# Performance work log

Hardware: AMD Instinct MI355X
Metric: run time of the kernel (lower is better)

## Reference

```python
import jax, jax.numpy as jnp
import numpy as np

N, F, H, E, R = 100000, 256, 64, 800000, 7
EPS = 1e-5

def _layernorm(x, g, b):
    mu = jnp.mean(x, axis=-1, keepdims=True)
    var = jnp.mean((x - mu) ** 2, axis=-1, keepdims=True)
    return (x - mu) * jax.lax.rsqrt(var + EPS) * g + b

def setup_inputs() -> dict:
    key = jax.random.key(0)
    ks = jax.random.split(key, 16)
    block_features = jax.random.normal(ks[0], (N, F), dtype=jnp.float32)
    src = jax.random.randint(ks[1], (E,), 0, N).astype(jnp.float32)
    dst = jax.random.randint(ks[2], (E,), 0, N).astype(jnp.float32)
    rel = jax.random.randint(ks[3], (E,), 0, R).astype(jnp.float32)
    w = jax.random.uniform(ks[4], (E,), dtype=jnp.float32)
    typed_edges = jnp.stack([src, dst, rel, w], axis=1)  # [E,4]
    def lin(k, fan_in, fan_out):
        s = 1.0 / np.sqrt(fan_in)
        k1, k2 = jax.random.split(k)
        return (jax.random.uniform(k1, (fan_in, fan_out), jnp.float32, -s, s),
                jax.random.uniform(k2, (fan_out,), jnp.float32, -s, s))
    W1, b1 = lin(ks[5], F, H)
    W2, b2 = lin(ks[6], H, H)
    rel_emb = jax.random.normal(ks[7], (R, H), dtype=jnp.float32)
    Wm1, bm1 = lin(ks[8], 3 * H + 1, H)
    Wm2, bm2 = lin(ks[9], H, H)
    Wg1, bg1 = lin(ks[10], 2 * H, H)
    Wg2, bg2 = lin(ks[11], H, H)
    return dict(block_features=block_features, typed_edges=typed_edges,
                W1=W1, b1=b1, g1=jnp.ones(H), be1=jnp.zeros(H), W2=W2, b2=b2,
                rel_emb=rel_emb, Wm1=Wm1, bm1=bm1, Wm2=Wm2, bm2=bm2,
                gn=jnp.ones(H), bn=jnp.zeros(H), Wg1=Wg1, bg1=bg1, Wg2=Wg2, bg2=bg2)

def reference(block_features, typed_edges, W1, b1, g1, be1, W2, b2, rel_emb,
              Wm1, bm1, Wm2, bm2, gn, bn, Wg1, bg1, Wg2, bg2):
    # node_proj: Linear -> LN -> ReLU -> Linear -> ReLU
    h = jax.nn.relu(_layernorm(block_features @ W1 + b1, g1, be1))
    h = jax.nn.relu(h @ W2 + b2)  # [N,H]
    src = typed_edges[:, 0].astype(jnp.int32)
    dst = typed_edges[:, 1].astype(jnp.int32)
    rel = typed_edges[:, 2].astype(jnp.int32)
    w = typed_edges[:, 3:4]  # [E,1]
    m_in = jnp.concatenate([h[src], h[dst], rel_emb[rel], w], axis=-1)  # [E,3H+1]
    msg = jax.nn.relu(m_in @ Wm1 + bm1) @ Wm2 + bm2  # [E,H]
    agg = jax.ops.segment_sum(msg, dst, num_segments=h.shape[0])  # [N,H]
    nodes = _layernorm(h + agg, gn, bn)
    g = jnp.concatenate([nodes.mean(axis=0), nodes.max(axis=0)], axis=-1)  # [2H]
    return jax.nn.relu(g @ Wg1 + bg1) @ Wg2 + bg2  # [H]
```

## Files before the change

kernel.cpp:

```cpp
#include <hip/hip_runtime.h>

typedef unsigned short u16;
typedef unsigned int   u32;
typedef __attribute__((ext_vector_type(8))) short bf16x8;
typedef __attribute__((ext_vector_type(4))) float f32x4;

#define EPS 1e-5f
#define MFMA(a,b,c) __builtin_amdgcn_mfma_f32_16x16x32_bf16(a,b,c,0,0,0)

constexpr int OB_b1=0, OB_g1=64, OB_be1=128, OB_b2=192, OB_bm1=256, OB_w192=320,
              OB_bm2=384, OB_gn=448, OB_bn=512, OB_bg1=576, OB_bg2=640,
              OB_Wg1=704, OB_Wg2=8896, WB_TOT=12992;
constexpr int FR_Wm1=0;
constexpr int FR_Wm2=12288;
constexpr int FR_rel=16384;
constexpr int FR_W1 =16960;
constexpr int FR_W2 =33344;
constexpr int FR_TOT=37440;

__device__ __forceinline__ float bf2f(u32 u) { return __uint_as_float(u << 16); }
__device__ __forceinline__ u16 f2bf(float f) {
  u32 b = __float_as_uint(f);
  return (u16)((b + 0x7fffu + ((b >> 16) & 1u)) >> 16);
}
__device__ __forceinline__ u32 fkey(float f) {
  u32 b = __float_as_uint(f);
  return (b & 0x80000000u) ? ~b : (b | 0x80000000u);
}

__launch_bounds__(256)
__global__ void k_prep(const float* __restrict__ W1, const float* __restrict__ b1,
                       const float* __restrict__ g1, const float* __restrict__ be1,
                       const float* __restrict__ W2, const float* __restrict__ b2,
                       const float* __restrict__ rel_emb,
                       const float* __restrict__ Wm1, const float* __restrict__ bm1,
                       const float* __restrict__ Wm2, const float* __restrict__ bm2,
                       const float* __restrict__ gn, const float* __restrict__ bn,
                       const float* __restrict__ Wg1, const float* __restrict__ bg1,
                       const float* __restrict__ Wg2, const float* __restrict__ bg2,
                       float* __restrict__ wbuf, u16* __restrict__ frags) {
  int tid = blockIdx.x * 256 + threadIdx.x;
  int nth = gridDim.x * 256;
  for (int i = tid; i < 64; i += nth) {
    wbuf[OB_b1 + i] = b1[i];   wbuf[OB_g1 + i] = g1[i];
    wbuf[OB_be1 + i] = be1[i]; wbuf[OB_b2 + i] = b2[i];
    wbuf[OB_bm1 + i] = bm1[i]; wbuf[OB_w192 + i] = Wm1[192 * 64 + i];
    wbuf[OB_bm2 + i] = bm2[i]; wbuf[OB_gn + i] = gn[i];
    wbuf[OB_bn + i] = bn[i];   wbuf[OB_bg1 + i] = bg1[i];
    wbuf[OB_bg2 + i] = bg2[i];
  }
  for (int i = tid; i < 8192; i += nth) wbuf[OB_Wg1 + i] = Wg1[i];
  for (int i = tid; i < 4096; i += nth) wbuf[OB_Wg2 + i] = Wg2[i];
  for (int idx = tid; idx < 16384; idx += nth) {
    int f = idx >> 9, L = (idx >> 3) & 63, j = idx & 7;
    int k = (f >> 2) * 32 + ((L >> 4) << 3) + j, n = ((f & 3) << 4) + (L & 15);
    frags[FR_W1 + idx] = f2bf(W1[k * 64 + n]);
  }
  for (int idx = tid; idx < 4096; idx += nth) {
    int f = idx >> 9, L = (idx >> 3) & 63, j = idx & 7;
    int k = (f >> 2) * 32 + ((L >> 4) << 3) + j, n = ((f & 3) << 4) + (L & 15);
    frags[FR_W2 + idx] = f2bf(W2[k * 64 + n]);
  }
  for (int idx = tid; idx < 12288; idx += nth) {
    int f = idx >> 9, L = (idx >> 3) & 63, j = idx & 7;
    int k = (f >> 2) * 32 + ((L >> 4) << 3) + j, n = ((f & 3) << 4) + (L & 15);
    frags[FR_Wm1 + idx] = f2bf(Wm1[k * 64 + n]);
  }
  for (int idx = tid; idx < 4096; idx += nth) {
    int f = idx >> 9, L = (idx >> 3) & 63, j = idx & 7;
    int k = (f >> 2) * 32 + ((L >> 4) << 3) + j, n = ((f & 3) << 4) + (L & 15);
    frags[FR_Wm2 + idx] = f2bf(Wm2[k * 64 + n]);
  }
  for (int idx = tid; idx < 576; idx += nth) {
    int r = idx / 80, c = idx % 80;
    frags[FR_rel + idx] = (r < 7 && c < 64) ? f2bf(rel_emb[r * 64 + c]) : (u16)0;
  }
}

__launch_bounds__(256, 3)
__global__ void k_h(const float* __restrict__ X, const float* __restrict__ wbuf,
                    const u16* __restrict__ frags, u16* __restrict__ hb, int N) {
  __shared__ __align__(16) u16 sW1[32 * 512];
  __shared__ __align__(16) u16 sW2[8 * 512];
  __shared__ __align__(16) u16 st[4][16 * 72];

  {
    const uint4* srcp = (const uint4*)(frags + FR_W1);
    uint4* d1 = (uint4*)sW1;
    for (int i = threadIdx.x; i < 2048; i += 256) d1[i] = srcp[i];
    const uint4* srcp2 = (const uint4*)(frags + FR_W2);
    uint4* d2 = (uint4*)sW2;
    for (int i = threadIdx.x; i < 512; i += 256) d2[i] = srcp2[i];
  }
  __syncthreads();

  int lane = threadIdx.x & 63, wave = threadIdx.x >> 6;
  int m = lane & 15, quad = lane >> 4, koff = quad * 8, col0 = m;

  float b1v[4], g1v[4], be1v[4], b2v[4];
  #pragma unroll
  for (int nt = 0; nt < 4; nt++) {
    int c = nt * 16 + col0;
    b1v[nt] = wbuf[OB_b1 + c]; g1v[nt] = wbuf[OB_g1 + c];
    be1v[nt] = wbuf[OB_be1 + c]; b2v[nt] = wbuf[OB_b2 + c];
  }

  int ntiles = (N + 15) / 16;
  int wid = blockIdx.x * 4 + wave, nw = gridDim.x * 4;
  for (int tile = wid; tile < ntiles; tile += nw) {
    int n0 = tile * 16;
    int nm = min(n0 + m, N - 1);
    const float* xr = X + (size_t)nm * 256 + koff;

    f32x4 acc[4] = {};
    #pragma unroll 1
    for (int ks = 0; ks < 8; ks++) {
      float4 u0 = *(const float4*)(xr + ks * 32);
      float4 u1 = *(const float4*)(xr + ks * 32 + 4);
      bf16x8 a;
      a[0] = (short)f2bf(u0.x); a[1] = (short)f2bf(u0.y);
      a[2] = (short)f2bf(u0.z); a[3] = (short)f2bf(u0.w);
      a[4] = (short)f2bf(u1.x); a[5] = (short)f2bf(u1.y);
      a[6] = (short)f2bf(u1.z); a[7] = (short)f2bf(u1.w);
      #pragma unroll
      for (int nt = 0; nt < 4; nt++) {
        bf16x8 b = *(const bf16x8*)(sW1 + (ks * 4 + nt) * 512 + lane * 8);
        acc[nt] = MFMA(a, b, acc[nt]);
      }
    }

    float v[4][4];
    #pragma unroll
    for (int nt = 0; nt < 4; nt++)
      #pragma unroll
      for (int r = 0; r < 4; r++) v[nt][r] = acc[nt][r] + b1v[nt];

    #pragma unroll
    for (int r = 0; r < 4; r++) {
      float s = v[0][r] + v[1][r] + v[2][r] + v[3][r];
      #pragma unroll
      for (int mk = 8; mk >= 1; mk >>= 1) s += __shfl_xor(s, mk, 64);
      float mu = s * (1.f / 64.f);
      float q = 0.f;
      #pragma unroll
      for (int nt = 0; nt < 4; nt++) { float d = v[nt][r] - mu; q += d * d; }
      #pragma unroll
      for (int mk = 8; mk >= 1; mk >>= 1) q += __shfl_xor(q, mk, 64);
      float rs = rsqrtf(q * (1.f / 64.f) + EPS);
      #pragma unroll
      for (int nt = 0; nt < 4; nt++) {
        float h1 = fmaxf(fmaf((v[nt][r] - mu) * rs, g1v[nt], be1v[nt]), 0.f);
        st[wave][(quad * 4 + r) * 72 + nt * 16 + col0] = f2bf(h1);
      }
    }
    __builtin_amdgcn_wave_barrier();

    f32x4 acc2[4] = {};
    #pragma unroll
    for (int ks = 0; ks < 2; ks++) {
      bf16x8 a2 = *(const bf16x8*)(st[wave] + m * 72 + ks * 32 + koff);
      #pragma unroll
      for (int nt = 0; nt < 4; nt++) {
        bf16x8 b = *(const bf16x8*)(sW2 + (ks * 4 + nt) * 512 + lane * 8);
        acc2[nt] = MFMA(a2, b, acc2[nt]);
      }
    }
    __builtin_amdgcn_wave_barrier();

    #pragma unroll
    for (int nt = 0; nt < 4; nt++)
      #pragma unroll
      for (int r = 0; r < 4; r++) {
        int row = n0 + quad * 4 + r;
        if (row < N)
          hb[(size_t)row * 64 + nt * 16 + col0] = f2bf(fmaxf(acc2[nt][r] + b2v[nt], 0.f));
      }
  }
}

__launch_bounds__(256, 3)
__global__ void k_edge(const float* __restrict__ te, const u16* __restrict__ hb,
                       const float* __restrict__ wbuf, const u16* __restrict__ frags,
                       float* __restrict__ agg, int E, int N) {
  __shared__ __align__(16) u16 sWm1[24 * 512];
  __shared__ __align__(16) u16 sWm2[8 * 512];
  __shared__ __align__(16) u16 srel[576];
  __shared__ __align__(16) u16 st[4][16 * 72];

  {
    const uint4* s1 = (const uint4*)(frags + FR_Wm1);
    uint4* d1 = (uint4*)sWm1;
    for (int i = threadIdx.x; i < 1536; i += 256) d1[i] = s1[i];
    const uint4* s2 = (const uint4*)(frags + FR_Wm2);
    uint4* d2 = (uint4*)sWm2;
    for (int i = threadIdx.x; i < 512; i += 256) d2[i] = s2[i];
    const uint4* s3 = (const uint4*)(frags + FR_rel);
    uint4* d3 = (uint4*)srel;
    for (int i = threadIdx.x; i < 72; i += 256) d3[i] = s3[i];
  }
  __syncthreads();

  int lane = threadIdx.x & 63, wave = threadIdx.x >> 6;
  int m = lane & 15, quad = lane >> 4, koff = quad * 8, col0 = m;

  float bm1v[4], w192v[4], bm2v[4];
  #pragma unroll
  for (int nt = 0; nt < 4; nt++) {
    int c = nt * 16 + col0;
    bm1v[nt] = wbuf[OB_bm1 + c];
    w192v[nt] = wbuf[OB_w192 + c];
    bm2v[nt] = wbuf[OB_bm2 + c];
  }

  int ntiles = (E + 15) / 16;
  int wid = blockIdx.x * 4 + wave, nw = gridDim.x * 4;
  for (int tile = wid; tile < ntiles; tile += nw) {
    int e0 = tile * 16;
    int src = 0, dst = 0, rel = 0; float w = 0.f;
    if (lane < 16) {
      int e = min(e0 + lane, E - 1);
      float4 v = *(const float4*)(te + (size_t)e * 4);
      src = min(max((int)v.x, 0), N - 1);
      dst = min(max((int)v.y, 0), N - 1);
      rel = min(max((int)v.z, 0), 6);
      w = v.w;
    }
    int src_m = __shfl(src, m, 64);
    int dst_m = __shfl(dst, m, 64);
    int rel_m = __shfl(rel, m, 64);

    const u16* hs = hb + (size_t)src_m * 64;
    const u16* hd = hb + (size_t)dst_m * 64;
    bf16x8 af[6];
    af[0] = *(const bf16x8*)(hs + koff);
    af[1] = *(const bf16x8*)(hs + 32 + koff);
    af[2] = *(const bf16x8*)(hd + koff);
    af[3] = *(const bf16x8*)(hd + 32 + koff);
    af[4] = *(const bf16x8*)(srel + rel_m * 80 + koff);
    af[5] = *(const bf16x8*)(srel + rel_m * 80 + 32 + koff);

    f32x4 acc[4] = {};
    #pragma unroll
    for (int ks = 0; ks < 6; ks++) {
      #pragma unroll
      for (int nt = 0; nt < 4; nt++) {
        bf16x8 b = *(const bf16x8*)(sWm1 + (ks * 4 + nt) * 512 + lane * 8);
        acc[nt] = MFMA(af[ks], b, acc[nt]);
      }
    }

    float wrow[4];
    #pragma unroll
    for (int r = 0; r < 4; r++) wrow[r] = __shfl(w, quad * 4 + r, 64);
    #pragma unroll
    for (int nt = 0; nt < 4; nt++)
      #pragma unroll
      for (int r = 0; r < 4; r++) {
        float v = fmaf(wrow[r], w192v[nt], acc[nt][r] + bm1v[nt]);
        st[wave][(quad * 4 + r) * 72 + nt * 16 + col0] = f2bf(fmaxf(v, 0.f));
      }
    __builtin_amdgcn_wave_barrier();

    f32x4 acc2[4] = {};
    #pragma unroll
    for (int ks = 0; ks < 2; ks++) {
      bf16x8 a2 = *(const bf16x8*)(st[wave] + m * 72 + ks * 32 + koff);
      #pragma unroll
      for (int nt = 0; nt < 4; nt++) {
        bf16x8 b = *(const bf16x8*)(sWm2 + (ks * 4 + nt) * 512 + lane * 8);
        acc2[nt] = MFMA(a2, b, acc2[nt]);
      }
    }
    __builtin_amdgcn_wave_barrier();

    int dstr[4]; bool valr[4];
    #pragma unroll
    for (int r = 0; r < 4; r++) {
      int row = quad * 4 + r;
      dstr[r] = __shfl(dst, row, 64);
      valr[r] = (e0 + row) < E;
    }
    #pragma unroll
    for (int nt = 0; nt < 4; nt++)
      #pragma unroll
      for (int r = 0; r < 4; r++)
        if (valr[r])
          atomicAdd(agg + (size_t)dstr[r] * 64 + nt * 16 + col0, acc2[nt][r] + bm2v[nt]);
  }
}

__launch_bounds__(256)
__global__ void k_nodes(const u16* __restrict__ hb, const float* __restrict__ agg,
                        const float* __restrict__ wbuf, float* __restrict__ gsum,
                        u32* __restrict__ gmax, int N) {
  int lane = threadIdx.x & 63, wave = threadIdx.x >> 6;
  int wid = blockIdx.x * 4 + wave;
  int nw = gridDim.x * 4;
  float gn = wbuf[OB_gn + lane], bn = wbuf[OB_bn + lane];
  float sj = 0.f, mj = -3.0e38f;
  for (int n = wid; n < N; n += nw) {
    float v = bf2f(hb[(size_t)n * 64 + lane]) + agg[(size_t)n * 64 + lane];
    float s = v;
    #pragma unroll
    for (int m = 32; m >= 1; m >>= 1) s += __shfl_xor(s, m, 64);
    float mu = s * (1.f / 64.f);
    float d = v - mu;
    float q = d * d;
    #pragma unroll
    for (int m = 32; m >= 1; m >>= 1) q += __shfl_xor(q, m, 64);
    float rs = rsqrtf(q * (1.f / 64.f) + EPS);
    float val = fmaf(d * rs, gn, bn);
    sj += val;
    mj = fmaxf(mj, val);
  }
  __shared__ float bs[256], bm[256];
  bs[threadIdx.x] = sj;
  bm[threadIdx.x] = mj;
  __syncthreads();
  if (threadIdx.x < 64) {
    int t = threadIdx.x;
    float ts = bs[t] + bs[64 + t] + bs[128 + t] + bs[192 + t];
    float tm = fmaxf(fmaxf(bm[t], bm[64 + t]), fmaxf(bm[128 + t], bm[192 + t]));
    atomicAdd(gsum + t, ts);
    atomicMax(gmax + t, fkey(tm));
  }
}

__launch_bounds__(128)
__global__ void k_final(const float* __restrict__ wbuf, const float* __restrict__ gsum,
                        const u32* __restrict__ gmax, float* __restrict__ out, int N) {
  __shared__ float g[128];
  __shared__ float y1[64];
  int t = threadIdx.x;
  if (t < 64) {
    g[t] = gsum[t] / (float)N;
  } else {
    u32 k = gmax[t - 64];
    u32 b = (k & 0x80000000u) ? (k & 0x7fffffffu) : ~k;
    g[t] = __uint_as_float(b);
  }
  __syncthreads();
  if (t < 64) {
    float a = wbuf[OB_bg1 + t];
    for (int i = 0; i < 128; i++) a = fmaf(g[i], wbuf[OB_Wg1 + i * 64 + t], a);
    y1[t] = fmaxf(a, 0.f);
  }
  __syncthreads();
  if (t < 64) {
    float a = wbuf[OB_bg2 + t];
    for (int k = 0; k < 64; k++) a = fmaf(y1[k], wbuf[OB_Wg2 + k * 64 + t], a);
    out[t] = a;
  }
}

extern "C" void kernel_launch(void* const* d_in, const int* in_sizes, int n_in,
                              void* d_out, int out_size, void* d_ws, size_t ws_size,
                              hipStream_t stream) {
  const int N = in_sizes[0] / 256;
  const int E = in_sizes[1] / 4;

  char* ws = (char*)d_ws;
  size_t aggB = (size_t)N * 64 * 4;
  size_t hbB  = (size_t)N * 64 * 2;
  float* agg   = (float*)ws;
  u16*   hb    = (u16*)(ws + aggB);
  float* gsum  = (float*)(ws + aggB + hbB);
  u32*   gmax  = (u32*)(ws + aggB + hbB + 256);
  float* wbuf  = (float*)(ws + aggB + hbB + 512);
  u16*   frags = (u16*)(ws + aggB + hbB + 512 + (size_t)WB_TOT * 4);

  const float* X  = (const float*)d_in[0];
  const float* te = (const float*)d_in[1];

  hipLaunchKernelGGL(k_prep, dim3(64), dim3(256), 0, stream,
                     (const float*)d_in[2], (const float*)d_in[3], (const float*)d_in[4],
                     (const float*)d_in[5], (const float*)d_in[6], (const float*)d_in[7],
                     (const float*)d_in[8], (const float*)d_in[9], (const float*)d_in[10],
                     (const float*)d_in[11], (const float*)d_in[12], (const float*)d_in[13],
                     (const float*)d_in[14], (const float*)d_in[15], (const float*)d_in[16],
                     (const float*)d_in[17], (const float*)d_in[18], wbuf, frags);
  hipMemsetAsync(agg, 0, aggB, stream);
  hipMemsetAsync(gsum, 0, 512, stream);
  hipLaunchKernelGGL(k_h, dim3(640), dim3(256), 0, stream, X, wbuf, frags, hb, N);
  hipLaunchKernelGGL(k_edge, dim3(768), dim3(256), 0, stream, te, hb, wbuf, frags, agg, E, N);
  hipLaunchKernelGGL(k_nodes, dim3(2048), dim3(256), 0, stream, hb, agg, wbuf, gsum, gmax, N);
  hipLaunchKernelGGL(k_final, dim3(1), dim3(128), 0, stream, wbuf, gsum, gmax, (float*)d_out, N);
}
```

Before: 442.6 us.

## Sort edges by destination and reduce messages per segment before atomics

Adds a counting sort of edges by destination: a count pass in the prep kernel, a three-kernel scan and a permutation kernel. The edge kernel then walks sorted ranges of 128 edges, adding up messages for each destination inside the wave. It writes interior segments with plain stores and uses atomics only for segments that touch a range boundary. The goal is to cut the roughly 64 fp32 atomics issued per edge. In exchange it adds extra launches, random reads of the edge table through the permutation, a serial 16-row reduction loop, and rounding of message outputs to bf16 before they are summed. It also unrolls the node-projection K loop and changes grid sizes.

```diff
diff --git a/kernel.cpp b/kernel.cpp
--- a/kernel.cpp
+++ b/kernel.cpp
@@ -38,7 +38,9 @@
                        const float* __restrict__ gn, const float* __restrict__ bn,
                        const float* __restrict__ Wg1, const float* __restrict__ bg1,
                        const float* __restrict__ Wg2, const float* __restrict__ bg2,
-                       float* __restrict__ wbuf, u16* __restrict__ frags) {
+                       float* __restrict__ wbuf, u16* __restrict__ frags,
+                       const float* __restrict__ te, u32* __restrict__ counts,
+                       int E, int N) {
   int tid = blockIdx.x * 256 + threadIdx.x;
   int nth = gridDim.x * 256;
   for (int i = tid; i < 64; i += nth) {
@@ -75,6 +77,76 @@
     int r = idx / 80, c = idx % 80;
     frags[FR_rel + idx] = (r < 7 && c < 64) ? f2bf(rel_emb[r * 64 + c]) : (u16)0;
   }
+  for (int e = tid; e < E; e += nth) {
+    float dv = te[(size_t)e * 4 + 1];
+    int d = min(max((int)dv, 0), N - 1);
+    atomicAdd(&counts[d], 1u);
+  }
+}
+
+__launch_bounds__(256)
+__global__ void k_scan1(const u32* __restrict__ counts, u32* __restrict__ partial, int M) {
+  __shared__ u32 red[256];
+  int base = blockIdx.x * 1024;
+  u32 s = 0;
+  #pragma unroll
+  for (int k = 0; k < 4; k++) { int i = base + threadIdx.x + k * 256; if (i < M) s += counts[i]; }
+  red[threadIdx.x] = s; __syncthreads();
+  for (int off = 128; off > 0; off >>= 1) {
+    if (threadIdx.x < (u32)off) red[threadIdx.x] += red[threadIdx.x + off];
+    __syncthreads();
+  }
+  if (threadIdx.x == 0) partial[blockIdx.x] = red[0];
+}
+
+__launch_bounds__(256)
+__global__ void k_scan2(u32* __restrict__ partial, int PB) {
+  __shared__ u32 sh[1024];
+  for (int i = threadIdx.x; i < PB; i += 256) sh[i] = partial[i];
+  __syncthreads();
+  if (threadIdx.x == 0) {
+    u32 acc = 0;
+    for (int i = 0; i < PB; i++) { u32 t = sh[i]; sh[i] = acc; acc += t; }
+  }
+  __syncthreads();
+  for (int i = threadIdx.x; i < PB; i += 256) partial[i] = sh[i];
+}
+
+__launch_bounds__(256)
+__global__ void k_scan3(const u32* __restrict__ counts, const u32* __restrict__ partial,
+                        u32* __restrict__ offsets, u32* __restrict__ cursor, int M) {
+  __shared__ u32 tsum[256];
+  int base = blockIdx.x * 1024 + threadIdx.x * 4;
+  u32 c[4]; u32 s = 0;
+  #pragma unroll
+  for (int k = 0; k < 4; k++) { int i = base + k; c[k] = (i < M) ? counts[i] : 0u; s += c[k]; }
+  tsum[threadIdx.x] = s; __syncthreads();
+  for (int off = 1; off < 256; off <<= 1) {
+    u32 v = (threadIdx.x >= (u32)off) ? tsum[threadIdx.x - off] : 0u;
+    __syncthreads();
+    tsum[threadIdx.x] += v;
+    __syncthreads();
+  }
+  u32 excl = (threadIdx.x == 0) ? 0u : tsum[threadIdx.x - 1];
+  u32 run = partial[blockIdx.x] + excl;
+  #pragma unroll
+  for (int k = 0; k < 4; k++) {
+    int i = base + k;
+    if (i < M) { offsets[i] = run; cursor[i] = run; run += c[k]; }
+  }
+}
+
+__launch_bounds__(256)
+__global__ void k_perm(const float* __restrict__ te, u32* __restrict__ cursor,
+                       u32* __restrict__ perm, int E, int N) {
+  int tid = blockIdx.x * 256 + threadIdx.x;
+  int nth = gridDim.x * 256;
+  for (int e = tid; e < E; e += nth) {
+    float dv = te[(size_t)e * 4 + 1];
+    int d = min(max((int)dv, 0), N - 1);
+    u32 pos = atomicAdd(&cursor[d], 1u);
+    perm[pos] = (u32)e;
+  }
 }
 
 __launch_bounds__(256, 3)
@@ -113,7 +185,7 @@
     const float* xr = X + (size_t)nm * 256 + koff;
 
     f32x4 acc[4] = {};
-    #pragma unroll 1
+    #pragma unroll 4
     for (int ks = 0; ks < 8; ks++) {
       float4 u0 = *(const float4*)(xr + ks * 32);
       float4 u1 = *(const float4*)(xr + ks * 32 + 4);
@@ -179,13 +251,15 @@
 }
 
 __launch_bounds__(256, 3)
-__global__ void k_edge(const float* __restrict__ te, const u16* __restrict__ hb,
-                       const float* __restrict__ wbuf, const u16* __restrict__ frags,
-                       float* __restrict__ agg, int E, int N) {
+__global__ void k_edge(const float* __restrict__ te, const u32* __restrict__ perm,
+                       const u16* __restrict__ hb, const float* __restrict__ wbuf,
+                       const u16* __restrict__ frags, float* __restrict__ agg,
+                       int E, int N, int nranges) {
   __shared__ __align__(16) u16 sWm1[24 * 512];
   __shared__ __align__(16) u16 sWm2[8 * 512];
   __shared__ __align__(16) u16 srel[576];
   __shared__ __align__(16) u16 st[4][16 * 72];
+  __shared__ int ldst[4][16];
 
   {
     const uint4* s1 = (const uint4*)(frags + FR_Wm1);
@@ -212,80 +286,105 @@
     bm2v[nt] = wbuf[OB_bm2 + c];
   }
 
-  int ntiles = (E + 15) / 16;
   int wid = blockIdx.x * 4 + wave, nw = gridDim.x * 4;
-  for (int tile = wid; tile < ntiles; tile += nw) {
-    int e0 = tile * 16;
-    int src = 0, dst = 0, rel = 0; float w = 0.f;
-    if (lane < 16) {
-      int e = min(e0 + lane, E - 1);
-      float4 v = *(const float4*)(te + (size_t)e * 4);
-      src = min(max((int)v.x, 0), N - 1);
-      dst = min(max((int)v.y, 0), N - 1);
-      rel = min(max((int)v.z, 0), 6);
-      w = v.w;
+  for (int range = wid; range < nranges; range += nw) {
+    int r0 = range * 128;
+    int run_dst = -2;
+    float run = 0.f;
+    bool bs = false;
+
+    #pragma unroll 1
+    for (int t8 = 0; t8 < 8; t8++) {
+      int p0 = r0 + t8 * 16;
+      if (p0 >= E) break;
+
+      int src = 0, dstc = 0, rel = 0, dtag = -1; float w = 0.f;
+      if (lane < 16) {
+        int p = p0 + lane;
+        if (p < E) {
+          u32 eid = perm[p];
+          float4 v = *(const float4*)(te + (size_t)eid * 4);
+          src = min(max((int)v.x, 0), N - 1);
+          dstc = min(max((int)v.y, 0), N - 1);
+          rel = min(max((int)v.z, 0), 6);
+          w = v.w;
+          dtag = dstc;
+        }
+        ldst[wave][lane] = dtag;
+      }
+      int src_m = __shfl(src, m, 64);
+      int dst_m = __shfl(dstc, m, 64);
+      int rel_m = __shfl(rel, m, 64);
+
+      const u16* hs = hb + (size_t)src_m * 64;
+      const u16* hd = hb + (size_t)dst_m * 64;
+      bf16x8 af[6];
+      af[0] = *(const bf16x8*)(hs + koff);
+      af[1] = *(const bf16x8*)(hs + 32 + koff);
+      af[2] = *(const bf16x8*)(hd + koff);
+      af[3] = *(const bf16x8*)(hd + 32 + koff);
+      af[4] = *(const bf16x8*)(srel + rel_m * 80 + koff);
+      af[5] = *(const bf16x8*)(srel + rel_m * 80 + 32 + koff);
+
+      f32x4 acc[4] = {};
+      #pragma unroll
+      for (int ks = 0; ks < 6; ks++) {
+        #pragma unroll
+        for (int nt = 0; nt < 4; nt++) {
+          bf16x8 b = *(const bf16x8*)(sWm1 + (ks * 4 + nt) * 512 + lane * 8);
+          acc[nt] = MFMA(af[ks], b, acc[nt]);
+        }
+      }
+
+      float wrow[4];
+      #pragma unroll
+      for (int r = 0; r < 4; r++) wrow[r] = __shfl(w, quad * 4 + r, 64);
+      #pragma unroll
+      for (int nt = 0; nt < 4; nt++)
+        #pragma unroll
+        for (int r = 0; r < 4; r++) {
+          float v = fmaf(wrow[r], w192v[nt], acc[nt][r] + bm1v[nt]);
+          st[wave][(quad * 4 + r) * 72 + nt * 16 + col0] = f2bf(fmaxf(v, 0.f));
+        }
+      __builtin_amdgcn_wave_barrier();
+
+      f32x4 acc2[4] = {};
+      #pragma unroll
+      for (int ks = 0; ks < 2; ks++) {
+        bf16x8 a2 = *(const bf16x8*)(st[wave] + m * 72 + ks * 32 + koff);
+        #pragma unroll
+        for (int nt = 0; nt < 4; nt++) {
+          bf16x8 b = *(const bf16x8*)(sWm2 + (ks * 4 + nt) * 512 + lane * 8);
+          acc2[nt] = MFMA(a2, b, acc2[nt]);
+        }
+      }
+      __builtin_amdgcn_wave_barrier();
+
+      #pragma unroll
+      for (int nt = 0; nt < 4; nt++)
+        #pragma unroll
+        for (int r = 0; r < 4; r++)
+          st[wave][(quad * 4 + r) * 72 + nt * 16 + col0] =
+              f2bf(acc2[nt][r] + bm2v[nt]);
+      __builtin_amdgcn_wave_barrier();
+
+      #pragma unroll 1
+      for (int r = 0; r < 16; r++) {
+        int d = ldst[wave][r];
+        float val = bf2f(st[wave][r * 72 + lane]);
+        if (d != run_dst) {
+          if (run_dst >= 0) {
+            float* ap = agg + (size_t)run_dst * 64 + lane;
+            if (bs) atomicAdd(ap, run); else *ap = run;
+          }
+          run_dst = d; run = val; bs = (t8 == 0 && r == 0);
+        } else {
+          run += val;
+        }
+      }
+      __builtin_amdgcn_wave_barrier();
     }
-    int src_m = __shfl(src, m, 64);
-    int dst_m = __shfl(dst, m, 64);
-    int rel_m = __shfl(rel, m, 64);
-
-    const u16* hs = hb + (size_t)src_m * 64;
-    const u16* hd = hb + (size_t)dst_m * 64;
-    bf16x8 af[6];
-    af[0] = *(const bf16x8*)(hs + koff);
-    af[1] = *(const bf16x8*)(hs + 32 + koff);
-    af[2] = *(const bf16x8*)(hd + koff);
-    af[3] = *(const bf16x8*)(hd + 32 + koff);
-    af[4] = *(const bf16x8*)(srel + rel_m * 80 + koff);
-    af[5] = *(const bf16x8*)(srel + rel_m * 80 + 32 + koff);
-
-    f32x4 acc[4] = {};
-    #pragma unroll
-    for (int ks = 0; ks < 6; ks++) {
-      #pragma unroll
-      for (int nt = 0; nt < 4; nt++) {
-        bf16x8 b = *(const bf16x8*)(sWm1 + (ks * 4 + nt) * 512 + lane * 8);
-        acc[nt] = MFMA(af[ks], b, acc[nt]);
-      }
-    }
-
-    float wrow[4];
-    #pragma unroll
-    for (int r = 0; r < 4; r++) wrow[r] = __shfl(w, quad * 4 + r, 64);
-    #pragma unroll
-    for (int nt = 0; nt < 4; nt++)
-      #pragma unroll
-      for (int r = 0; r < 4; r++) {
-        float v = fmaf(wrow[r], w192v[nt], acc[nt][r] + bm1v[nt]);
-        st[wave][(quad * 4 + r) * 72 + nt * 16 + col0] = f2bf(fmaxf(v, 0.f));
-      }
-    __builtin_amdgcn_wave_barrier();
-
-    f32x4 acc2[4] = {};
-    #pragma unroll
-    for (int ks = 0; ks < 2; ks++) {
-      bf16x8 a2 = *(const bf16x8*)(st[wave] + m * 72 + ks * 32 + koff);
-      #pragma unroll
-      for (int nt = 0; nt < 4; nt++) {
-        bf16x8 b = *(const bf16x8*)(sWm2 + (ks * 4 + nt) * 512 + lane * 8);
-        acc2[nt] = MFMA(a2, b, acc2[nt]);
-      }
-    }
-    __builtin_amdgcn_wave_barrier();
-
-    int dstr[4]; bool valr[4];
-    #pragma unroll
-    for (int r = 0; r < 4; r++) {
-      int row = quad * 4 + r;
-      dstr[r] = __shfl(dst, row, 64);
-      valr[r] = (e0 + row) < E;
-    }
-    #pragma unroll
-    for (int nt = 0; nt < 4; nt++)
-      #pragma unroll
-      for (int r = 0; r < 4; r++)
-        if (valr[r])
-          atomicAdd(agg + (size_t)dstr[r] * 64 + nt * 16 + col0, acc2[nt][r] + bm2v[nt]);
+    if (run_dst >= 0) atomicAdd(agg + (size_t)run_dst * 64 + lane, run);
   }
 }
 
@@ -358,31 +457,44 @@
                               hipStream_t stream) {
   const int N = in_sizes[0] / 256;
   const int E = in_sizes[1] / 4;
+  const int M = N + 1;
+  const int Mp = (M + 63) & ~63;
+  const int PB = (M + 1023) / 1024;
 
   char* ws = (char*)d_ws;
-  size_t aggB = (size_t)N * 64 * 4;
-  size_t hbB  = (size_t)N * 64 * 2;
-  float* agg   = (float*)ws;
-  u16*   hb    = (u16*)(ws + aggB);
-  float* gsum  = (float*)(ws + aggB + hbB);
-  u32*   gmax  = (u32*)(ws + aggB + hbB + 256);
-  float* wbuf  = (float*)(ws + aggB + hbB + 512);
-  u16*   frags = (u16*)(ws + aggB + hbB + 512 + (size_t)WB_TOT * 4);
+  float* agg    = (float*)ws;
+  float* gsum   = agg + (size_t)N * 64;
+  u32*   gmax   = (u32*)(gsum + 64);
+  u32*   counts = gmax + 64;
+  size_t zeroB  = (size_t)N * 64 * 4 + 512 + (size_t)Mp * 4;
+  u32*   offsets = counts + Mp;
+  u32*   cursor  = offsets + Mp;
+  u32*   partial = cursor + Mp;
+  u32*   perm    = partial + 256;
+  u16*   hb      = (u16*)(perm + ((E + 7) & ~7));
+  float* wbuf    = (float*)(hb + (size_t)N * 64);
+  u16*   frags   = (u16*)(wbuf + WB_TOT);
 
   const float* X  = (const float*)d_in[0];
   const float* te = (const float*)d_in[1];
 
-  hipLaunchKernelGGL(k_prep, dim3(64), dim3(256), 0, stream,
+  hipMemsetAsync(agg, 0, zeroB, stream);
+  hipLaunchKernelGGL(k_prep, dim3(400), dim3(256), 0, stream,
                      (const float*)d_in[2], (const float*)d_in[3], (const float*)d_in[4],
                      (const float*)d_in[5], (const float*)d_in[6], (const float*)d_in[7],
                      (const float*)d_in[8], (const float*)d_in[9], (const float*)d_in[10],
                      (const float*)d_in[11], (const float*)d_in[12], (const float*)d_in[13],
                      (const float*)d_in[14], (const float*)d_in[15], (const float*)d_in[16],
-                     (const float*)d_in[17], (const float*)d_in[18], wbuf, frags);
-  hipMemsetAsync(agg, 0, aggB, stream);
-  hipMemsetAsync(gsum, 0, 512, stream);
-  hipLaunchKernelGGL(k_h, dim3(640), dim3(256), 0, stream, X, wbuf, frags, hb, N);
-  hipLaunchKernelGGL(k_edge, dim3(768), dim3(256), 0, stream, te, hb, wbuf, frags, agg, E, N);
+                     (const float*)d_in[17], (const float*)d_in[18], wbuf, frags,
+                     te, counts, E, N);
+  hipLaunchKernelGGL(k_scan1, dim3(PB), dim3(256), 0, stream, counts, partial, M);
+  hipLaunchKernelGGL(k_scan2, dim3(1), dim3(256), 0, stream, partial, PB);
+  hipLaunchKernelGGL(k_scan3, dim3(PB), dim3(256), 0, stream, counts, partial, offsets, cursor, M);
+  hipLaunchKernelGGL(k_perm, dim3(800), dim3(256), 0, stream, te, cursor, perm, E, N);
+  hipLaunchKernelGGL(k_h, dim3(800), dim3(256), 0, stream, X, wbuf, frags, hb, N);
+  int nranges = (E + 127) / 128;
+  hipLaunchKernelGGL(k_edge, dim3(768), dim3(256), 0, stream,
+                     te, perm, hb, wbuf, frags, agg, E, N, nranges);
   hipLaunchKernelGGL(k_nodes, dim3(2048), dim3(256), 0, stream, hb, agg, wbuf, gsum, gmax, N);
   hipLaunchKernelGGL(k_final, dim3(1), dim3(128), 0, stream, wbuf, gsum, gmax, (float*)d_out, N);
 }
```

Measured after the change: 459.9 us. 3.9% more time.
